# Kernel tuning notes

Measured on AMD Instinct MI355X. Metric: run time of the kernel, lower is better.

Reference implementation:

```python
import jax, jax.numpy as jnp
import numpy as np

TAU = 0.1
EPS_FREQ = 1e-06
EPS_DENOM = 1e-12


def _l2norm(x, eps=1e-12):
    # matches F.normalize(p=2, dim=-1)
    n = jnp.linalg.norm(x, axis=-1, keepdims=True)
    return x / jnp.maximum(n, eps)


def setup_inputs() -> dict:
    key = jax.random.key(0)
    k1, k2, k3, k4, k5 = jax.random.split(key, 5)
    N, D, C = 4096, 128, 64
    return {
        "protos": jax.random.normal(k1, (C, D), dtype=jnp.float32),
        "proj2": jax.random.normal(k2, (N, D), dtype=jnp.float32),
        "target2": jax.random.randint(k3, (N,), 0, C, dtype=jnp.int64),
        "proj3": jax.random.normal(k4, (N, D), dtype=jnp.float32),
        "target3": jax.random.randint(k5, (N,), 0, C, dtype=jnp.int64),
    }


def reference(protos, proj2, target2, proj3, target3):
    feats = _l2norm(jnp.concatenate([proj2, proj3], axis=0))        # [M, D]
    labels = jnp.concatenate([target2, target3], axis=0)             # [M]
    protos_n = _l2norm(protos)                                       # [C, D]
    M = feats.shape[0]
    C = protos_n.shape[0]

    sim = jnp.matmul(feats, feats.T) / TAU                           # [M, M]
    proto_sim = jnp.matmul(feats, protos_n.T) / TAU                  # [M, C]

    eye = jnp.eye(M, dtype=bool)
    exp_sim = jnp.where(eye, 0.0, jnp.exp(sim))                      # diag masked to -inf -> exp 0
    exp_proto = jnp.exp(proto_sim)

    match = labels[:, None] == labels[None, :]                       # [M, M]
    numer_region = jnp.sum(exp_sim * match, axis=1)                  # [M]
    numer_proto = jnp.take_along_axis(exp_proto, labels[:, None], axis=1)[:, 0]
    numer = numer_region + numer_proto

    # bincount(labels ++ arange(C)) == per-class count + 1
    cls_freq = jnp.zeros((C,), dtype=jnp.float32).at[labels].add(1.0) + 1.0 + EPS_FREQ
    feat_w = cls_freq[labels]                                        # [M], per-row weight

    denom_region = jnp.sum(exp_sim, axis=1) / feat_w                 # row-constant weight; diag already 0
    denom_proto = jnp.sum(exp_proto / cls_freq[None, :], axis=1)
    denom = denom_region + denom_proto

    loss = -jnp.log(numer / (denom + EPS_DENOM))
    return jnp.mean(loss)
```

## Files before the change

### kernel.cpp

```cpp
#include <hip/hip_runtime.h>
#include <math.h>
#include <stdint.h>

#define D    128
#define CCLS 64
#define CH   16
#define HB   8

typedef _Float16 f16x8 __attribute__((ext_vector_type(8)));
typedef float    f32x4 __attribute__((ext_vector_type(4)));

__device__ __forceinline__ float wave_reduce_sum(float v) {
    #pragma unroll
    for (int off = 32; off > 0; off >>= 1) v += __shfl_xor(v, off, 64);
    return v;
}

__device__ __forceinline__ void gload_lds16(const void* g, void* l) {
    __builtin_amdgcn_global_load_lds(
        (const __attribute__((address_space(1))) uint32_t*)g,
        (__attribute__((address_space(3))) uint32_t*)l, 16, 0, 0);
}
__device__ __forceinline__ void gload_lds4(const void* g, void* l) {
    __builtin_amdgcn_global_load_lds(
        (const __attribute__((address_space(1))) uint32_t*)g,
        (__attribute__((address_space(3))) uint32_t*)l, 4, 0, 0);
}

__global__ void norm_kernel(const float* __restrict__ protos,
                            const float* __restrict__ proj2,
                            const float* __restrict__ proj3,
                            const int* __restrict__ t2, const int* __restrict__ t3,
                            _Float16* __restrict__ ftile, int* __restrict__ labs,
                            float* __restrict__ hpart, float* __restrict__ loss_sum,
                            int* __restrict__ ticket, int N, int M) {
    const float SCL = 3.8017368953f;
    int w = threadIdx.x >> 6;
    int lane = threadIdx.x & 63;
    int row = blockIdx.x * (blockDim.x >> 6) + w;
    const int MT = M + 128;

    if (blockIdx.x < HB) {
        __shared__ int h[CCLS];
        int t = threadIdx.x;
        if (t < CCLS) h[t] = 0;
        __syncthreads();
        int base = blockIdx.x * (M / HB);
        for (int i = t; i < M / HB; i += (int)blockDim.x) {
            int gi = base + i;
            int lab = (gi < N) ? t2[gi] : t3[gi - N];
            atomicAdd(&h[lab], 1);
        }
        __syncthreads();
        if (t < CCLS) hpart[blockIdx.x * CCLS + t] = (float)h[t];
    }
    if (blockIdx.x == HB && threadIdx.x == 0) { loss_sum[0] = 0.f; ticket[0] = 0; }

    if (row < MT) {
        const float* src = nullptr;
        if (row < M)             src = (row < N) ? proj2 + (size_t)row * D
                                                 : proj3 + (size_t)(row - N) * D;
        else if (row < M + CCLS) src = protos + (size_t)(row - M) * D;
        float2 v = {0.f, 0.f};
        if (src) v = ((const float2*)src)[lane];
        float ss = wave_reduce_sum(v.x * v.x + v.y * v.y);
        float scale = src ? SCL / fmaxf(sqrtf(ss), 1e-12f) : 0.f;
        _Float16 h0 = (_Float16)(v.x * scale), h1 = (_Float16)(v.y * scale);
        int k0 = 2 * lane;
        size_t off = ((size_t)(row >> 4) * 16 + (k0 >> 3)) * 128 + (row & 15) * 8 + (k0 & 7);
        ftile[off] = h0; ftile[off + 1] = h1;
        if (row < M && lane == 0)
            labs[row] = (row < N) ? t2[row] : t3[row - N];
    }
}

__global__ __launch_bounds__(256, 4)
void sim_kernel(const _Float16* __restrict__ ftile,
                const int* __restrict__ labs,
                const float* __restrict__ hpart,
                float* __restrict__ nPart, float* __restrict__ dPart,
                float* __restrict__ rp, int M) {
    __shared__ _Float16 bbuf[3][4096];
    __shared__ int labL[512];

    const int panel = blockIdx.x;
    const int chunk = blockIdx.y;
    const int t = threadIdx.x;
    const int w = t >> 6, lane = t & 63;
    const int g = lane >> 4, li = lane & 15;
    const int lo = g * 128 + li * 8;
    const int rtA = panel * 8 + w * 2;
    const int nH = 16;
    const int sBase = chunk * 8;
    const int row0 = panel * 128 + 32 * w + li;
    const int rl0 = labs[row0];
    const int rl1 = labs[row0 + 16];

    f16x8 a[2][4];
    #pragma unroll
    for (int m = 0; m < 2; ++m)
        #pragma unroll
        for (int kt = 0; kt < 4; ++kt)
            a[m][kt] = *(const f16x8*)(ftile + (size_t)(rtA + m) * 2048 + kt * 512 + lo);

    float rn[2] = {0.f, 0.f}, rd[2] = {0.f, 0.f};

    {
        const char* lsrc = (const char*)labs + (size_t)sBase * 256;
        #pragma unroll
        for (int c = 0; c < 2; ++c) {
            int cc = w * 2 + c;
            gload_lds4(lsrc + cc * 256 + lane * 4, (char*)labL + cc * 256);
        }
    }
    #define STAGE_H(buf, h)                                                       \
        {                                                                         \
            const char* src_ = (const char*)ftile + (size_t)sBase * 16384         \
                               + (size_t)(h) * 8192;                              \
            char* dst_ = (char*)&bbuf[(buf)][0];                                  \
            _Pragma("unroll")                                                     \
            for (int c = 0; c < 2; ++c) {                                         \
                int j_ = w * 2 + c;                                               \
                gload_lds16(src_ + (size_t)j_ * 1024 + lane * 16,                 \
                            dst_ + (size_t)j_ * 1024);                            \
            }                                                                     \
        }
    STAGE_H(0, 0);
    STAGE_H(1, 1);

    const int diagS = 2 * panel + (w >> 1);
    const int nD0 = 2 * (w & 1);

    for (int h = 0; h < nH; ++h) {
        if (h < nH - 1) { asm volatile("s_waitcnt vmcnt(2)" ::: "memory"); }
        else            { asm volatile("s_waitcnt vmcnt(0)" ::: "memory"); }
        __builtin_amdgcn_s_barrier();

        const _Float16* Bl = &bbuf[h % 3][0];
        const int s = sBase + (h >> 1);
        const bool isDiag = (s == diagS);
        const int nBase = (h & 1) * 2;

        #pragma unroll
        for (int nl = 0; nl < 2; ++nl) {
            f16x8 bn[4];
            #pragma unroll
            for (int kt = 0; kt < 4; ++kt)
                bn[kt] = *(const f16x8*)(Bl + nl * 2048 + kt * 512 + lo);

            f32x4 acc[2];
            #pragma unroll
            for (int m = 0; m < 2; ++m)
                #pragma unroll
                for (int r = 0; r < 4; ++r) acc[m][r] = 0.f;

            #pragma unroll
            for (int kt = 0; kt < 4; ++kt)
                #pragma unroll
                for (int m = 0; m < 2; ++m)
                    acc[m] = __builtin_amdgcn_mfma_f32_16x16x32_f16(bn[kt], a[m][kt], acc[m], 0, 0, 0);

            if (isDiag) {
                #pragma unroll
                for (int m = 0; m < 2; ++m)
                    #pragma unroll
                    for (int r = 0; r < 4; ++r)
                        acc[m][r] = (nBase + nl == nD0 + m && 4 * g + r == li)
                                    ? -1e5f : acc[m][r];
            }

            int4 c4 = *(const int4*)(labL + h * 32 + nl * 16 + 4 * g);
            #pragma unroll
            for (int m = 0; m < 2; ++m) {
                float e0 = __builtin_amdgcn_exp2f(acc[m][0]);
                float e1 = __builtin_amdgcn_exp2f(acc[m][1]);
                float e2 = __builtin_amdgcn_exp2f(acc[m][2]);
                float e3 = __builtin_amdgcn_exp2f(acc[m][3]);
                const int rl = m ? rl1 : rl0;
                rd[m] += e0 + e1 + e2 + e3;
                rn[m] += (c4.x == rl) ? e0 : 0.f;
                rn[m] += (c4.y == rl) ? e1 : 0.f;
                rn[m] += (c4.z == rl) ? e2 : 0.f;
                rn[m] += (c4.w == rl) ? e3 : 0.f;
            }
        }

        if (h + 2 < nH) STAGE_H((h + 2) % 3, h + 2);
    }

    float rpacc[2] = {0.f, 0.f};
    if (chunk == 0) {
        const int rbp = M >> 4;
        #pragma unroll
        for (int n = 0; n < 4; ++n) {
            f16x8 bn[4];
            #pragma unroll
            for (int kt = 0; kt < 4; ++kt)
                bn[kt] = *(const f16x8*)(ftile + (size_t)(rbp + n) * 2048 + kt * 512 + lo);
            f32x4 acc[2];
            #pragma unroll
            for (int m = 0; m < 2; ++m)
                #pragma unroll
                for (int r = 0; r < 4; ++r) acc[m][r] = 0.f;
            #pragma unroll
            for (int kt = 0; kt < 4; ++kt)
                #pragma unroll
                for (int m = 0; m < 2; ++m)
                    acc[m] = __builtin_amdgcn_mfma_f32_16x16x32_f16(bn[kt], a[m][kt], acc[m], 0, 0, 0);

            f32x4 fr = {1.0f + 1e-6f, 1.0f + 1e-6f, 1.0f + 1e-6f, 1.0f + 1e-6f};
            #pragma unroll
            for (int b = 0; b < HB; ++b)
                fr += *(const f32x4*)(hpart + b * CCLS + 16 * n + 4 * g);
            const int c0 = 16 * n + 4 * g;
            #pragma unroll
            for (int m = 0; m < 2; ++m) {
                float e0 = __builtin_amdgcn_exp2f(acc[m][0]);
                float e1 = __builtin_amdgcn_exp2f(acc[m][1]);
                float e2 = __builtin_amdgcn_exp2f(acc[m][2]);
                float e3 = __builtin_amdgcn_exp2f(acc[m][3]);
                const int rl = m ? rl1 : rl0;
                rpacc[m] += e0 / fr[0] + e1 / fr[1] + e2 / fr[2] + e3 / fr[3];
                rn[m] += (c0 + 0 == rl) ? e0 : 0.f;
                rn[m] += (c0 + 1 == rl) ? e1 : 0.f;
                rn[m] += (c0 + 2 == rl) ? e2 : 0.f;
                rn[m] += (c0 + 3 == rl) ? e3 : 0.f;
            }
        }
    }

    #pragma unroll
    for (int m = 0; m < 2; ++m) {
        rn[m] += __shfl_xor(rn[m], 16, 64); rn[m] += __shfl_xor(rn[m], 32, 64);
        rd[m] += __shfl_xor(rd[m], 16, 64); rd[m] += __shfl_xor(rd[m], 32, 64);
        if (chunk == 0) {
            rpacc[m] += __shfl_xor(rpacc[m], 16, 64);
            rpacc[m] += __shfl_xor(rpacc[m], 32, 64);
        }
    }
    if (lane < 16) {
        #pragma unroll
        for (int m = 0; m < 2; ++m) {
            const int rowm = row0 + 16 * m;
            nPart[(size_t)chunk * M + rowm] = rn[m];
            dPart[(size_t)chunk * M + rowm] = rd[m];
            if (chunk == 0) rp[rowm] = rpacc[m];
        }
    }
}

__global__ void fin_kernel(const int* __restrict__ labs,
                           const float* __restrict__ hpart,
                           const float* __restrict__ nPart,
                           const float* __restrict__ dPart,
                           const float* __restrict__ rp,
                           float* __restrict__ loss_sum, int* __restrict__ ticket,
                           float* __restrict__ out, int M) {
    int i = blockIdx.x * blockDim.x + threadIdx.x;
    float l = 0.f;
    if (i < M) {
        float rnT = 0.f, rdT = 0.f;
        #pragma unroll
        for (int ch = 0; ch < CH; ++ch) {
            rnT += nPart[(size_t)ch * M + i];
            rdT += dPart[(size_t)ch * M + i];
        }
        int lab = labs[i];
        float fsum = 1.0f + 1e-6f;
        #pragma unroll
        for (int b = 0; b < HB; ++b) fsum += hpart[b * CCLS + lab];
        float denom = rdT / fsum + rp[i];
        l = logf(denom + 1e-12f) - logf(rnT);
    }
    l = wave_reduce_sum(l);
    __shared__ float ws_[4];
    if ((threadIdx.x & 63) == 0) ws_[threadIdx.x >> 6] = l;
    __syncthreads();
    if (threadIdx.x == 0) {
        atomicAdd(loss_sum, ws_[0] + ws_[1] + ws_[2] + ws_[3]);
        __threadfence();
        int old = atomicAdd(ticket, 1);
        if (old == (int)gridDim.x - 1) {
            __threadfence();
            out[0] = *(volatile float*)loss_sum / (float)M;
        }
    }
}

extern "C" void kernel_launch(void* const* d_in, const int* in_sizes, int n_in,
                              void* d_out, int out_size, void* d_ws, size_t ws_size,
                              hipStream_t stream) {
    const float* protos = (const float*)d_in[0];
    const float* proj2  = (const float*)d_in[1];
    const int*   t2     = (const int*)d_in[2];
    const float* proj3  = (const float*)d_in[3];
    const int*   t3     = (const int*)d_in[4];
    float* out = (float*)d_out;

    const int N = in_sizes[1] / D;
    const int M = 2 * N;
    const int MT = M + 128;

    _Float16* ftile = (_Float16*)d_ws;
    int*   labs     = (int*)(ftile + (size_t)MT * D);
    float* hpart    = (float*)(labs + M);
    float* nPart    = hpart + HB * CCLS;
    float* dPart    = nPart + (size_t)CH * M;
    float* rp       = dPart + (size_t)CH * M;
    float* loss_sum = rp + M;
    int*   ticket   = (int*)(loss_sum + 1);

    norm_kernel<<<(MT + 3) / 4, 256, 0, stream>>>(protos, proj2, proj3, t2, t3,
                                                  ftile, labs, hpart, loss_sum,
                                                  ticket, N, M);
    dim3 grid(M / 128, CH);
    sim_kernel<<<grid, 256, 0, stream>>>(ftile, labs, hpart, nPart, dPart, rp, M);
    fin_kernel<<<(M + 255) / 256, 256, 0, stream>>>(labs, hpart, nPart, dPart, rp,
                                                    loss_sum, ticket, out, M);
}
```

Before: 37.65 us.

## Exploit similarity symmetry with upper-triangular 128x128 tile grid

Replaces the full panel-by-chunk grid with one block per upper-triangular 128x128 tile pair, computing each off-diagonal tile once and producing both row and column partial sums via shuffle and LDS reductions. This roughly halves the MFMA and exp work. The B tile is now loaded whole into LDS instead of being triple-buffered, and the finalize kernel sums P=64 partials per row instead of 16. The trade-off is larger partial buffers, extra column-reduction shuffles and LDS traffic, and a loop-based triangular index decode.

```diff
diff --git a/kernel.cpp b/kernel.cpp
--- a/kernel.cpp
+++ b/kernel.cpp
@@ -4,7 +4,6 @@
 
 #define D    128
 #define CCLS 64
-#define CH   16
 #define HB   8
 
 typedef _Float16 f16x8 __attribute__((ext_vector_type(8)));
@@ -20,11 +19,6 @@
     __builtin_amdgcn_global_load_lds(
         (const __attribute__((address_space(1))) uint32_t*)g,
         (__attribute__((address_space(3))) uint32_t*)l, 16, 0, 0);
-}
-__device__ __forceinline__ void gload_lds4(const void* g, void* l) {
-    __builtin_amdgcn_global_load_lds(
-        (const __attribute__((address_space(1))) uint32_t*)g,
-        (__attribute__((address_space(3))) uint32_t*)l, 4, 0, 0);
 }
 
 __global__ void norm_kernel(const float* __restrict__ protos,
@@ -80,22 +74,32 @@
                 const float* __restrict__ hpart,
                 float* __restrict__ nPart, float* __restrict__ dPart,
                 float* __restrict__ rp, int M) {
-    __shared__ _Float16 bbuf[3][4096];
-    __shared__ int labL[512];
-
-    const int panel = blockIdx.x;
-    const int chunk = blockIdx.y;
+    __shared__ __align__(16) _Float16 Bl[16384];
+    __shared__ int labL[128];
+    __shared__ float colp[4][2][4][32];
+
+    const int P = M / 128;
+    int b = blockIdx.x, pi = 0, rem = P;
+    while (b >= rem) { b -= rem; --rem; ++pi; }
+    const int pj = pi + b;
+    const bool diagB = (pi == pj);
+
     const int t = threadIdx.x;
     const int w = t >> 6, lane = t & 63;
     const int g = lane >> 4, li = lane & 15;
     const int lo = g * 128 + li * 8;
-    const int rtA = panel * 8 + w * 2;
-    const int nH = 16;
-    const int sBase = chunk * 8;
-    const int row0 = panel * 128 + 32 * w + li;
-    const int rl0 = labs[row0];
-    const int rl1 = labs[row0 + 16];
-
+
+    {
+        const char* src = (const char*)(ftile + (size_t)pj * 16384);
+        char* dst = (char*)Bl;
+        #pragma unroll
+        for (int q = 0; q < 8; ++q)
+            gload_lds16(src + (size_t)(w * 8 + q) * 1024 + lane * 16,
+                        dst + (size_t)(w * 8 + q) * 1024);
+    }
+    if (t >= 128) labL[t - 128] = labs[pj * 128 + (t - 128)];
+
+    const int rtA = pi * 8 + w * 2;
     f16x8 a[2][4];
     #pragma unroll
     for (int m = 0; m < 2; ++m)
@@ -103,93 +107,81 @@
         for (int kt = 0; kt < 4; ++kt)
             a[m][kt] = *(const f16x8*)(ftile + (size_t)(rtA + m) * 2048 + kt * 512 + lo);
 
+    const int row0 = pi * 128 + 32 * w + li;
+    const int rl0 = labs[row0];
+    const int rl1 = labs[row0 + 16];
     float rn[2] = {0.f, 0.f}, rd[2] = {0.f, 0.f};
 
-    {
-        const char* lsrc = (const char*)labs + (size_t)sBase * 256;
-        #pragma unroll
-        for (int c = 0; c < 2; ++c) {
-            int cc = w * 2 + c;
-            gload_lds4(lsrc + cc * 256 + lane * 4, (char*)labL + cc * 256);
-        }
-    }
-    #define STAGE_H(buf, h)                                                       \
-        {                                                                         \
-            const char* src_ = (const char*)ftile + (size_t)sBase * 16384         \
-                               + (size_t)(h) * 8192;                              \
-            char* dst_ = (char*)&bbuf[(buf)][0];                                  \
-            _Pragma("unroll")                                                     \
-            for (int c = 0; c < 2; ++c) {                                         \
-                int j_ = w * 2 + c;                                               \
-                gload_lds16(src_ + (size_t)j_ * 1024 + lane * 16,                 \
-                            dst_ + (size_t)j_ * 1024);                            \
-            }                                                                     \
-        }
-    STAGE_H(0, 0);
-    STAGE_H(1, 1);
-
-    const int diagS = 2 * panel + (w >> 1);
-    const int nD0 = 2 * (w & 1);
-
-    for (int h = 0; h < nH; ++h) {
-        if (h < nH - 1) { asm volatile("s_waitcnt vmcnt(2)" ::: "memory"); }
-        else            { asm volatile("s_waitcnt vmcnt(0)" ::: "memory"); }
-        __builtin_amdgcn_s_barrier();
-
-        const _Float16* Bl = &bbuf[h % 3][0];
-        const int s = sBase + (h >> 1);
-        const bool isDiag = (s == diagS);
-        const int nBase = (h & 1) * 2;
-
-        #pragma unroll
-        for (int nl = 0; nl < 2; ++nl) {
-            f16x8 bn[4];
-            #pragma unroll
-            for (int kt = 0; kt < 4; ++kt)
-                bn[kt] = *(const f16x8*)(Bl + nl * 2048 + kt * 512 + lo);
-
-            f32x4 acc[2];
+    __syncthreads();
+
+    #pragma unroll
+    for (int n = 0; n < 8; ++n) {
+        f16x8 bn[4];
+        #pragma unroll
+        for (int kt = 0; kt < 4; ++kt)
+            bn[kt] = *(const f16x8*)(Bl + n * 2048 + kt * 512 + lo);
+
+        f32x4 acc[2];
+        #pragma unroll
+        for (int m = 0; m < 2; ++m)
+            #pragma unroll
+            for (int r = 0; r < 4; ++r) acc[m][r] = 0.f;
+
+        #pragma unroll
+        for (int kt = 0; kt < 4; ++kt)
             #pragma unroll
             for (int m = 0; m < 2; ++m)
-                #pragma unroll
-                for (int r = 0; r < 4; ++r) acc[m][r] = 0.f;
-
-            #pragma unroll
-            for (int kt = 0; kt < 4; ++kt)
-                #pragma unroll
-                for (int m = 0; m < 2; ++m)
-                    acc[m] = __builtin_amdgcn_mfma_f32_16x16x32_f16(bn[kt], a[m][kt], acc[m], 0, 0, 0);
-
-            if (isDiag) {
-                #pragma unroll
-                for (int m = 0; m < 2; ++m)
-                    #pragma unroll
-                    for (int r = 0; r < 4; ++r)
-                        acc[m][r] = (nBase + nl == nD0 + m && 4 * g + r == li)
-                                    ? -1e5f : acc[m][r];
+                acc[m] = __builtin_amdgcn_mfma_f32_16x16x32_f16(bn[kt], a[m][kt], acc[m], 0, 0, 0);
+
+        if (diagB) {
+            #pragma unroll
+            for (int m = 0; m < 2; ++m)
+                #pragma unroll
+                for (int r = 0; r < 4; ++r)
+                    acc[m][r] = (n == 2 * w + m && 4 * g + r == li) ? -1e5f : acc[m][r];
+        }
+
+        int4 c4 = *(const int4*)(labL + n * 16 + 4 * g);
+        float rcd[4] = {0.f, 0.f, 0.f, 0.f};
+        float rcn[4] = {0.f, 0.f, 0.f, 0.f};
+        #pragma unroll
+        for (int m = 0; m < 2; ++m) {
+            float e0 = __builtin_amdgcn_exp2f(acc[m][0]);
+            float e1 = __builtin_amdgcn_exp2f(acc[m][1]);
+            float e2 = __builtin_amdgcn_exp2f(acc[m][2]);
+            float e3 = __builtin_amdgcn_exp2f(acc[m][3]);
+            const int rl = m ? rl1 : rl0;
+            float s0 = (c4.x == rl) ? e0 : 0.f;
+            float s1 = (c4.y == rl) ? e1 : 0.f;
+            float s2 = (c4.z == rl) ? e2 : 0.f;
+            float s3 = (c4.w == rl) ? e3 : 0.f;
+            rd[m] += (e0 + e1) + (e2 + e3);
+            rn[m] += (s0 + s1) + (s2 + s3);
+            rcd[0] += e0; rcd[1] += e1; rcd[2] += e2; rcd[3] += e3;
+            rcn[0] += s0; rcn[1] += s1; rcn[2] += s2; rcn[3] += s3;
+        }
+
+        if (!diagB) {
+            #pragma unroll
+            for (int r = 0; r < 4; ++r) {
+                #pragma unroll
+                for (int off = 1; off < 16; off <<= 1) {
+                    rcd[r] += __shfl_xor(rcd[r], off, 64);
+                    rcn[r] += __shfl_xor(rcn[r], off, 64);
+                }
             }
-
-            int4 c4 = *(const int4*)(labL + h * 32 + nl * 16 + 4 * g);
-            #pragma unroll
-            for (int m = 0; m < 2; ++m) {
-                float e0 = __builtin_amdgcn_exp2f(acc[m][0]);
-                float e1 = __builtin_amdgcn_exp2f(acc[m][1]);
-                float e2 = __builtin_amdgcn_exp2f(acc[m][2]);
-                float e3 = __builtin_amdgcn_exp2f(acc[m][3]);
-                const int rl = m ? rl1 : rl0;
-                rd[m] += e0 + e1 + e2 + e3;
-                rn[m] += (c4.x == rl) ? e0 : 0.f;
-                rn[m] += (c4.y == rl) ? e1 : 0.f;
-                rn[m] += (c4.z == rl) ? e2 : 0.f;
-                rn[m] += (c4.w == rl) ? e3 : 0.f;
+            if (li == 0) {
+                #pragma unroll
+                for (int r = 0; r < 4; ++r) {
+                    colp[w][0][r][n * 4 + g] = rcd[r];
+                    colp[w][1][r][n * 4 + g] = rcn[r];
+                }
             }
         }
-
-        if (h + 2 < nH) STAGE_H((h + 2) % 3, h + 2);
     }
 
     float rpacc[2] = {0.f, 0.f};
-    if (chunk == 0) {
+    if (diagB) {
         const int rbp = M >> 4;
         #pragma unroll
         for (int n = 0; n < 4; ++n) {
@@ -210,8 +202,8 @@
 
             f32x4 fr = {1.0f + 1e-6f, 1.0f + 1e-6f, 1.0f + 1e-6f, 1.0f + 1e-6f};
             #pragma unroll
-            for (int b = 0; b < HB; ++b)
-                fr += *(const f32x4*)(hpart + b * CCLS + 16 * n + 4 * g);
+            for (int hb = 0; hb < HB; ++hb)
+                fr += *(const f32x4*)(hpart + hb * CCLS + 16 * n + 4 * g);
             const int c0 = 16 * n + 4 * g;
             #pragma unroll
             for (int m = 0; m < 2; ++m) {
@@ -233,7 +225,7 @@
     for (int m = 0; m < 2; ++m) {
         rn[m] += __shfl_xor(rn[m], 16, 64); rn[m] += __shfl_xor(rn[m], 32, 64);
         rd[m] += __shfl_xor(rd[m], 16, 64); rd[m] += __shfl_xor(rd[m], 32, 64);
-        if (chunk == 0) {
+        if (diagB) {
             rpacc[m] += __shfl_xor(rpacc[m], 16, 64);
             rpacc[m] += __shfl_xor(rpacc[m], 32, 64);
         }
@@ -242,10 +234,21 @@
         #pragma unroll
         for (int m = 0; m < 2; ++m) {
             const int rowm = row0 + 16 * m;
-            nPart[(size_t)chunk * M + rowm] = rn[m];
-            dPart[(size_t)chunk * M + rowm] = rd[m];
-            if (chunk == 0) rp[rowm] = rpacc[m];
-        }
+            nPart[(size_t)pj * M + rowm] = rn[m];
+            dPart[(size_t)pj * M + rowm] = rd[m];
+            if (diagB) rp[rowm] = rpacc[m];
+        }
+    }
+
+    __syncthreads();
+    if (!diagB && t < 128) {
+        const int j = t, nn = j >> 4, gg = (j >> 2) & 3, rr = j & 3;
+        float sd = colp[0][0][rr][nn * 4 + gg] + colp[1][0][rr][nn * 4 + gg]
+                 + colp[2][0][rr][nn * 4 + gg] + colp[3][0][rr][nn * 4 + gg];
+        float sn = colp[0][1][rr][nn * 4 + gg] + colp[1][1][rr][nn * 4 + gg]
+                 + colp[2][1][rr][nn * 4 + gg] + colp[3][1][rr][nn * 4 + gg];
+        dPart[(size_t)pi * M + pj * 128 + j] = sd;
+        nPart[(size_t)pi * M + pj * 128 + j] = sn;
     }
 }
 
@@ -257,18 +260,18 @@
                            float* __restrict__ loss_sum, int* __restrict__ ticket,
                            float* __restrict__ out, int M) {
     int i = blockIdx.x * blockDim.x + threadIdx.x;
+    const int P = M / 128;
     float l = 0.f;
     if (i < M) {
         float rnT = 0.f, rdT = 0.f;
-        #pragma unroll
-        for (int ch = 0; ch < CH; ++ch) {
-            rnT += nPart[(size_t)ch * M + i];
-            rdT += dPart[(size_t)ch * M + i];
+        for (int s = 0; s < P; ++s) {
+            rnT += nPart[(size_t)s * M + i];
+            rdT += dPart[(size_t)s * M + i];
         }
         int lab = labs[i];
         float fsum = 1.0f + 1e-6f;
         #pragma unroll
-        for (int b = 0; b < HB; ++b) fsum += hpart[b * CCLS + lab];
+        for (int hb = 0; hb < HB; ++hb) fsum += hpart[hb * CCLS + lab];
         float denom = rdT / fsum + rp[i];
         l = logf(denom + 1e-12f) - logf(rnT);
     }
@@ -300,21 +303,22 @@
     const int N = in_sizes[1] / D;
     const int M = 2 * N;
     const int MT = M + 128;
+    const int P = M / 128;
 
     _Float16* ftile = (_Float16*)d_ws;
     int*   labs     = (int*)(ftile + (size_t)MT * D);
     float* hpart    = (float*)(labs + M);
     float* nPart    = hpart + HB * CCLS;
-    float* dPart    = nPart + (size_t)CH * M;
-    float* rp       = dPart + (size_t)CH * M;
+    float* dPart    = nPart + (size_t)P * M;
+    float* rp       = dPart + (size_t)P * M;
     float* loss_sum = rp + M;
     int*   ticket   = (int*)(loss_sum + 1);
 
     norm_kernel<<<(MT + 3) / 4, 256, 0, stream>>>(protos, proj2, proj3, t2, t3,
                                                   ftile, labs, hpart, loss_sum,
                                                   ticket, N, M);
-    dim3 grid(M / 128, CH);
-    sim_kernel<<<grid, 256, 0, stream>>>(ftile, labs, hpart, nPart, dPart, rp, M);
+    sim_kernel<<<P * (P + 1) / 2, 256, 0, stream>>>(ftile, labs, hpart,
+                                                    nPart, dPart, rp, M);
     fin_kernel<<<(M + 255) / 256, 256, 0, stream>>>(labs, hpart, nPart, dPart, rp,
                                                     loss_sum, ticket, out, M);
 }
```

New measurement: 88.43 us. 2.35x slower.
